# Performance work log

Hardware: AMD Instinct MI355X
Metric: run time of the kernel (lower is better)

Reference implementation:

```python
import jax, jax.numpy as jnp
import numpy as np

N = 262144   # batch of states
D = 32       # in_dim

def setup_inputs() -> dict:
    key = jax.random.key(0)
    k1, k2 = jax.random.split(key)
    x = jax.random.normal(k1, (N, D), dtype=jnp.float32)
    # learned bilinear tensor W[k, i, j], as in nn.Parameter(Tensor(D, D, D))
    weight = jax.random.normal(k2, (D, D, D), dtype=jnp.float32) * (1.0 / np.sqrt(D))
    return {"x": x, "weight": weight}

def reference(x, weight):
    # torch: xBx = x @ W @ x.T -> (D, N, N); out = diagonal(xBx.permute(2,1,0)).t()
    # i.e. out[n, k] = sum_{i,j} x[n,i] * W[k,i,j] * x[n,j]
    # Compute the batched quadratic form directly, skipping the (D, N, N) tensor.
    xW = jnp.einsum('ni,kij->nkj', x, weight)   # (N, D, D) intermediate
    out = jnp.einsum('nkj,nj->nk', xW, x)       # (N, D)
    return out
```

## Files before the change

### kernel.cpp

```cpp
#include <hip/hip_runtime.h>


typedef _Float16 f16x2 __attribute__((ext_vector_type(2)));
typedef _Float16 f16x4 __attribute__((ext_vector_type(4)));
typedef _Float16 f16x8 __attribute__((ext_vector_type(8)));
typedef float    f32x16 __attribute__((ext_vector_type(16)));

static __device__ __forceinline__ unsigned int pk2_f16(float lo, float hi) {
    return __builtin_bit_cast(unsigned int, __builtin_amdgcn_cvt_pkrtz(lo, hi));
}
static __device__ __forceinline__ f16x2 u2h(unsigned int u) {
    return __builtin_bit_cast(f16x2, u);
}
static __device__ __forceinline__ unsigned short f16b(float f) {
    _Float16 h = (_Float16)f;
    return __builtin_bit_cast(unsigned short, h);
}

__global__ __launch_bounds__(256)
void prep_btab_sym(const float* __restrict__ W, unsigned short* __restrict__ bt) {
    __shared__ float Wlds[1024];
    const int k = blockIdx.x;
    const int t = threadIdx.x;
    {
        const float4* src = (const float4*)(W + k * 1024);
        ((float4*)Wlds)[t] = src[t];
    }
    __syncthreads();
    if (t < 66) {
        int n  = t >> 1;
        int lh = t & 1;
        int d  = (n == 32) ? 16 : (n >> 1);
        int q  = (n == 32) ? 0  : (n & 1);
        unsigned short v[8];
        #pragma unroll
        for (int b = 0; b < 8; ++b) {
            int i = q * 16 + lh * 8 + b;
            int j = (i + d) & 31;
            float s = (d == 0) ? Wlds[i * 32 + i]
                               : Wlds[i * 32 + j] + Wlds[j * 32 + i];
            v[b] = f16b(s);
        }
        uint4 pk;
        pk.x = (unsigned int)v[0] | ((unsigned int)v[1] << 16);
        pk.y = (unsigned int)v[2] | ((unsigned int)v[3] << 16);
        pk.z = (unsigned int)v[4] | ((unsigned int)v[5] << 16);
        pk.w = (unsigned int)v[6] | ((unsigned int)v[7] << 16);
        ((uint4*)bt)[n * 64 + k + lh * 32] = pk;
    }
}

#define XS 18

__global__ __launch_bounds__(512, 4)
void quadform_kernel(const float* __restrict__ x,
                     const unsigned short* __restrict__ bt_ws,
                     float* __restrict__ out) {
    __shared__ __align__(16) unsigned short btab[33 * 64 * 8];
    __shared__ __align__(16) unsigned int   xstage[512 * XS];

    const int tid  = threadIdx.x;
    const int lane = tid & 63;
    const int wave = tid >> 6;
    const int hi   = lane >> 5;
    const int rl   = lane & 31;
    const long blockrow = (long)blockIdx.x * 512;
    const long wrow = blockrow + wave * 64;

    const float4* xsrc = (const float4*)(x + blockrow * 32);
    float4 xg0 = xsrc[tid];
    float4 xg1 = xsrc[512 + tid];
    float4 xg2 = xsrc[1024 + tid];
    float4 xg3 = xsrc[1536 + tid];
    float4 xg4 = xsrc[2048 + tid];
    float4 xg5 = xsrc[2560 + tid];
    float4 xg6 = xsrc[3072 + tid];
    float4 xg7 = xsrc[3584 + tid];

    const uint4* bsrc = (const uint4*)bt_ws;
    uint4* bdst = (uint4*)btab;
    {
        uint4 b0 = bsrc[tid];
        uint4 b1 = bsrc[512 + tid];
        uint4 b2 = bsrc[1024 + tid];
        uint4 b3 = bsrc[1536 + tid];
        bdst[tid]        = b0;
        bdst[512 + tid]  = b1;
        bdst[1024 + tid] = b2;
        bdst[1536 + tid] = b3;
        if (tid < 64) bdst[2048 + tid] = bsrc[2048 + tid];
    }

    #pragma unroll
    for (int c = 0; c < 8; ++c) {
        float4 v = (c == 0) ? xg0 : (c == 1) ? xg1 : (c == 2) ? xg2 :
                   (c == 3) ? xg3 : (c == 4) ? xg4 : (c == 5) ? xg5 :
                   (c == 6) ? xg6 : xg7;
        int idx = c * 512 + tid;
        int row = idx >> 3;
        int sub = idx & 7;
        uint2 w2;
        w2.x = pk2_f16(v.x, v.y);
        w2.y = pk2_f16(v.z, v.w);
        *(uint2*)&xstage[row * XS + sub * 2] = w2;
    }
    __syncthreads();

    unsigned int ypk0[16], ypk1[16];
    {
        unsigned int xpk0[16], xpk1[16];
        const unsigned int* xr0 = &xstage[(wave * 64 + rl) * XS];
        const unsigned int* xr1 = &xstage[(wave * 64 + 32 + rl) * XS];
        #pragma unroll
        for (int c = 0; c < 4; ++c) {
            uint4 v0 = *(const uint4*)(xr0 + c * 4);
            uint4 v1 = *(const uint4*)(xr1 + c * 4);
            xpk0[c * 4 + 0] = v0.x; xpk0[c * 4 + 1] = v0.y;
            xpk0[c * 4 + 2] = v0.z; xpk0[c * 4 + 3] = v0.w;
            xpk1[c * 4 + 0] = v1.x; xpk1[c * 4 + 1] = v1.y;
            xpk1[c * 4 + 2] = v1.z; xpk1[c * 4 + 3] = v1.w;
        }
        #pragma unroll
        for (int c = 0; c < 16; ++c) {
            ypk0[c] = hi ? xpk0[(c + 4) & 15] : xpk0[c];
            ypk1[c] = hi ? xpk1[(c + 4) & 15] : xpk1[c];
        }
    }

    f32x16 accA, accB;
    #pragma unroll
    for (int e = 0; e < 16; ++e) { accA[e] = 0.0f; accB[e] = 0.0f; }

    #pragma unroll
    for (int s = 0; s < 33; ++s) {
        const int d   = (s == 32) ? 16 : (s >> 1);
        const int q8  = ((s == 32) ? 0 : (s & 1)) * 8;
        const int dh  = d >> 1;
        const bool od = (d & 1) != 0;
        f16x8 bfrag = *(const f16x8*)(&btab[(s * 64 + lane) * 8]);

        {
            f16x2 b0 = od ? u2h(__builtin_amdgcn_perm(ypk0[(q8 + 0 + dh + 1) & 15], ypk0[(q8 + 0 + dh) & 15], 0x05040302u)) : u2h(ypk0[(q8 + 0 + dh) & 15]);
            f16x2 b1 = od ? u2h(__builtin_amdgcn_perm(ypk0[(q8 + 1 + dh + 1) & 15], ypk0[(q8 + 1 + dh) & 15], 0x05040302u)) : u2h(ypk0[(q8 + 1 + dh) & 15]);
            f16x2 b2 = od ? u2h(__builtin_amdgcn_perm(ypk0[(q8 + 2 + dh + 1) & 15], ypk0[(q8 + 2 + dh) & 15], 0x05040302u)) : u2h(ypk0[(q8 + 2 + dh) & 15]);
            f16x2 b3 = od ? u2h(__builtin_amdgcn_perm(ypk0[(q8 + 3 + dh + 1) & 15], ypk0[(q8 + 3 + dh) & 15], 0x05040302u)) : u2h(ypk0[(q8 + 3 + dh) & 15]);
            f16x2 a0 = u2h(ypk0[q8 + 0]) * b0;
            f16x2 a1 = u2h(ypk0[q8 + 1]) * b1;
            f16x2 a2 = u2h(ypk0[q8 + 2]) * b2;
            f16x2 a3 = u2h(ypk0[q8 + 3]) * b3;
            f16x4 lo = __builtin_shufflevector(a0, a1, 0, 1, 2, 3);
            f16x4 hf = __builtin_shufflevector(a2, a3, 0, 1, 2, 3);
            f16x8 a  = __builtin_shufflevector(lo, hf, 0, 1, 2, 3, 4, 5, 6, 7);
            accA = __builtin_amdgcn_mfma_f32_32x32x16_f16(a, bfrag, accA, 0, 0, 0);
        }
        {
            f16x2 b0 = od ? u2h(__builtin_amdgcn_perm(ypk1[(q8 + 0 + dh + 1) & 15], ypk1[(q8 + 0 + dh) & 15], 0x05040302u)) : u2h(ypk1[(q8 + 0 + dh) & 15]);
            f16x2 b1 = od ? u2h(__builtin_amdgcn_perm(ypk1[(q8 + 1 + dh + 1) & 15], ypk1[(q8 + 1 + dh) & 15], 0x05040302u)) : u2h(ypk1[(q8 + 1 + dh) & 15]);
            f16x2 b2 = od ? u2h(__builtin_amdgcn_perm(ypk1[(q8 + 2 + dh + 1) & 15], ypk1[(q8 + 2 + dh) & 15], 0x05040302u)) : u2h(ypk1[(q8 + 2 + dh) & 15]);
            f16x2 b3 = od ? u2h(__builtin_amdgcn_perm(ypk1[(q8 + 3 + dh + 1) & 15], ypk1[(q8 + 3 + dh) & 15], 0x05040302u)) : u2h(ypk1[(q8 + 3 + dh) & 15]);
            f16x2 a0 = u2h(ypk1[q8 + 0]) * b0;
            f16x2 a1 = u2h(ypk1[q8 + 1]) * b1;
            f16x2 a2 = u2h(ypk1[q8 + 2]) * b2;
            f16x2 a3 = u2h(ypk1[q8 + 3]) * b3;
            f16x4 lo = __builtin_shufflevector(a0, a1, 0, 1, 2, 3);
            f16x4 hf = __builtin_shufflevector(a2, a3, 0, 1, 2, 3);
            f16x8 a  = __builtin_shufflevector(lo, hf, 0, 1, 2, 3, 4, 5, 6, 7);
            accB = __builtin_amdgcn_mfma_f32_32x32x16_f16(a, bfrag, accB, 0, 0, 0);
        }
    }

    float* ob0 = out + (wrow + 4 * hi) * 32 + rl;
    float* ob1 = ob0 + 32 * 32;
    #pragma unroll
    for (int e = 0; e < 16; ++e) {
        __builtin_nontemporal_store(accA[e], ob0 + (e & 3) * 32 + (e >> 2) * 256);
        __builtin_nontemporal_store(accB[e], ob1 + (e & 3) * 32 + (e >> 2) * 256);
    }
}

extern "C" void kernel_launch(void* const* d_in, const int* in_sizes, int n_in,
                              void* d_out, int out_size, void* d_ws, size_t ws_size,
                              hipStream_t stream) {
    const float* x = (const float*)d_in[0];
    const float* W = (const float*)d_in[1];
    float* out = (float*)d_out;
    unsigned short* bt = (unsigned short*)d_ws;

    prep_btab_sym<<<32, 256, 0, stream>>>(W, bt);
    int nrows = in_sizes[0] / 32;
    int grid  = nrows / 512;
    quadform_kernel<<<grid, 512, 0, stream>>>(x, bt, out);
}
```

Baseline: 22.81 us.

## Hold B fragments in registers and stage x per wave without block barrier

Each wave now loads all 33 symmetric-weight MFMA fragments straight from global memory into registers instead of a block-shared LDS table. It stages its own 64 rows of x in a private LDS slice, which removes the __syncthreads. Blocks shrink from 512 to 256 threads and launch bounds change to (256,2). This trades LDS traffic and the block barrier for 132 extra VGPRs per thread and redundant global (L2) reads of the table by every wave, which may reduce occupancy.

```diff
diff --git a/kernel.cpp b/kernel.cpp
--- a/kernel.cpp
+++ b/kernel.cpp
@@ -52,73 +52,61 @@
 
 #define XS 18
 
-__global__ __launch_bounds__(512, 4)
+__global__ __launch_bounds__(256, 2)
 void quadform_kernel(const float* __restrict__ x,
-                     const unsigned short* __restrict__ bt_ws,
+                     const uint4* __restrict__ bt,
                      float* __restrict__ out) {
-    __shared__ __align__(16) unsigned short btab[33 * 64 * 8];
-    __shared__ __align__(16) unsigned int   xstage[512 * XS];
+    __shared__ __align__(16) unsigned int xstage[256 * XS];
 
     const int tid  = threadIdx.x;
     const int lane = tid & 63;
     const int wave = tid >> 6;
     const int hi   = lane >> 5;
     const int rl   = lane & 31;
-    const long blockrow = (long)blockIdx.x * 512;
-    const long wrow = blockrow + wave * 64;
+    const long wrow = (long)blockIdx.x * 256 + wave * 64;
 
-    const float4* xsrc = (const float4*)(x + blockrow * 32);
-    float4 xg0 = xsrc[tid];
-    float4 xg1 = xsrc[512 + tid];
-    float4 xg2 = xsrc[1024 + tid];
-    float4 xg3 = xsrc[1536 + tid];
-    float4 xg4 = xsrc[2048 + tid];
-    float4 xg5 = xsrc[2560 + tid];
-    float4 xg6 = xsrc[3072 + tid];
-    float4 xg7 = xsrc[3584 + tid];
+    uint4 bf[33];
+    #pragma unroll
+    for (int s = 0; s < 33; ++s) bf[s] = bt[s * 64 + lane];
 
-    const uint4* bsrc = (const uint4*)bt_ws;
-    uint4* bdst = (uint4*)btab;
-    {
-        uint4 b0 = bsrc[tid];
-        uint4 b1 = bsrc[512 + tid];
-        uint4 b2 = bsrc[1024 + tid];
-        uint4 b3 = bsrc[1536 + tid];
-        bdst[tid]        = b0;
-        bdst[512 + tid]  = b1;
-        bdst[1024 + tid] = b2;
-        bdst[1536 + tid] = b3;
-        if (tid < 64) bdst[2048 + tid] = bsrc[2048 + tid];
-    }
+    const float4* xsrc = (const float4*)(x + wrow * 32);
+    float4 v0 = xsrc[lane];
+    float4 v1 = xsrc[64 + lane];
+    float4 v2 = xsrc[128 + lane];
+    float4 v3 = xsrc[192 + lane];
+    float4 v4 = xsrc[256 + lane];
+    float4 v5 = xsrc[320 + lane];
+    float4 v6 = xsrc[384 + lane];
+    float4 v7 = xsrc[448 + lane];
 
+    unsigned int* ws = &xstage[wave * 64 * XS];
     #pragma unroll
     for (int c = 0; c < 8; ++c) {
-        float4 v = (c == 0) ? xg0 : (c == 1) ? xg1 : (c == 2) ? xg2 :
-                   (c == 3) ? xg3 : (c == 4) ? xg4 : (c == 5) ? xg5 :
-                   (c == 6) ? xg6 : xg7;
-        int idx = c * 512 + tid;
+        float4 v = (c == 0) ? v0 : (c == 1) ? v1 : (c == 2) ? v2 :
+                   (c == 3) ? v3 : (c == 4) ? v4 : (c == 5) ? v5 :
+                   (c == 6) ? v6 : v7;
+        int idx = c * 64 + lane;
         int row = idx >> 3;
         int sub = idx & 7;
         uint2 w2;
         w2.x = pk2_f16(v.x, v.y);
         w2.y = pk2_f16(v.z, v.w);
-        *(uint2*)&xstage[row * XS + sub * 2] = w2;
+        *(uint2*)&ws[row * XS + sub * 2] = w2;
     }
-    __syncthreads();
 
     unsigned int ypk0[16], ypk1[16];
     {
         unsigned int xpk0[16], xpk1[16];
-        const unsigned int* xr0 = &xstage[(wave * 64 + rl) * XS];
-        const unsigned int* xr1 = &xstage[(wave * 64 + 32 + rl) * XS];
+        const unsigned int* xr0 = &ws[rl * XS];
+        const unsigned int* xr1 = &ws[(32 + rl) * XS];
         #pragma unroll
         for (int c = 0; c < 4; ++c) {
-            uint4 v0 = *(const uint4*)(xr0 + c * 4);
-            uint4 v1 = *(const uint4*)(xr1 + c * 4);
-            xpk0[c * 4 + 0] = v0.x; xpk0[c * 4 + 1] = v0.y;
-            xpk0[c * 4 + 2] = v0.z; xpk0[c * 4 + 3] = v0.w;
-            xpk1[c * 4 + 0] = v1.x; xpk1[c * 4 + 1] = v1.y;
-            xpk1[c * 4 + 2] = v1.z; xpk1[c * 4 + 3] = v1.w;
+            uint4 a = *(const uint4*)(xr0 + c * 4);
+            uint4 b = *(const uint4*)(xr1 + c * 4);
+            xpk0[c * 4 + 0] = a.x; xpk0[c * 4 + 1] = a.y;
+            xpk0[c * 4 + 2] = a.z; xpk0[c * 4 + 3] = a.w;
+            xpk1[c * 4 + 0] = b.x; xpk1[c * 4 + 1] = b.y;
+            xpk1[c * 4 + 2] = b.z; xpk1[c * 4 + 3] = b.w;
         }
         #pragma unroll
         for (int c = 0; c < 16; ++c) {
@@ -137,7 +125,7 @@
         const int q8  = ((s == 32) ? 0 : (s & 1)) * 8;
         const int dh  = d >> 1;
         const bool od = (d & 1) != 0;
-        f16x8 bfrag = *(const f16x8*)(&btab[(s * 64 + lane) * 8]);
+        f16x8 bfrag = __builtin_bit_cast(f16x8, bf[s]);
 
         {
             f16x2 b0 = od ? u2h(__builtin_amdgcn_perm(ypk0[(q8 + 0 + dh + 1) & 15], ypk0[(q8 + 0 + dh) & 15], 0x05040302u)) : u2h(ypk0[(q8 + 0 + dh) & 15]);
@@ -188,6 +176,6 @@
 
     prep_btab_sym<<<32, 256, 0, stream>>>(W, bt);
     int nrows = in_sizes[0] / 32;
-    int grid  = nrows / 512;
-    quadform_kernel<<<grid, 512, 0, stream>>>(x, bt, out);
+    int grid  = nrows / 256;
+    quadform_kernel<<<grid, 256, 0, stream>>>(x, (const uint4*)bt, out);
 }
```

New measurement: 24.81 us. 1.09x slower.
